# Performance work log

Hardware: AMD Instinct MI355X
Metric: run time of the kernel (lower is better)

The kernel has to match this reference:

```python
import jax, jax.numpy as jnp
import numpy as np

N = 50000   # nodes
E = 1000000 # edges
D_IN = 64
D_OUT = 64
R = 16      # relations (num_rels == num_bases)


def setup_inputs() -> dict:
    key = jax.random.key(0)
    k1, k2, k3, k4, k5, k6, k7 = jax.random.split(key, 7)
    node_features = jax.random.normal(k1, (N, D_IN), dtype=jnp.float32)
    edge_src = jax.random.randint(k2, (E,), 0, N, dtype=jnp.int32)
    edge_dst = jax.random.randint(k3, (E,), 0, N, dtype=jnp.int32)
    edge_type = jax.random.randint(k4, (E,), 0, R, dtype=jnp.int32)
    edge_norm = jax.random.uniform(k5, (E,), dtype=jnp.float32)
    weight = jax.random.normal(k6, (R, D_IN, D_OUT), dtype=jnp.float32) * 0.1
    bias = jax.random.normal(k7, (D_OUT,), dtype=jnp.float32) * 0.1
    return {
        "node_features": node_features,
        "edge_src": edge_src,
        "edge_dst": edge_dst,
        "edge_type": edge_type,
        "edge_norm": edge_norm,
        "weight": weight,
        "bias": bias,
    }


def reference(node_features, edge_src, edge_dst, edge_type, edge_norm, weight, bias):
    # gather source features and per-edge relation weight matrices
    h_src = node_features[edge_src]              # [E, D_IN]
    w = weight[edge_type]                        # [E, D_IN, D_OUT]
    # per-edge bmm: [E,1,D_IN] @ [E,D_IN,D_OUT] -> [E,D_OUT]
    msg = jnp.einsum('ed,edo->eo', h_src, w)
    msg = msg * edge_norm[:, None]               # norm scaling
    # scatter-sum aggregation over destination nodes
    node_repr = jax.ops.segment_sum(msg, edge_dst, num_segments=N)  # [N, D_OUT]
    node_repr = node_repr + bias
    return jax.nn.relu(node_repr)
```

## Files before the change

kernel.cpp:

```cpp
#include <hip/hip_runtime.h>
#include <hip/hip_bf16.h>


#define NN 50000
#define EE 1000000
#define RR 16
#define NBLK 256
#define EPB 3907
#define BSH 6
#define NBUK 782
#define NS (NBUK * NBLK)
#define SCAP 2048

typedef __attribute__((ext_vector_type(8))) short short8;
typedef __attribute__((ext_vector_type(4))) float f32x4;

static __device__ inline unsigned short f2bf(float f) {
  union { __hip_bfloat16 h; unsigned short u; } cv;
  cv.h = __float2bfloat16(f);
  return cv.u;
}
static __device__ inline float bf2f(unsigned short u) {
  union { unsigned i; float f; } cv;
  cv.i = ((unsigned)u) << 16;
  return cv.f;
}

__global__ __launch_bounds__(256) void k_wt(const float* __restrict__ W,
                                            unsigned short* __restrict__ Wt) {
  __shared__ __align__(16) unsigned short Wl[64][72];
  const int r = blockIdx.x, tid = threadIdx.x;
  for (int i = tid; i < 4096; i += 256) Wl[i & 63][i >> 6] = f2bf(W[(r << 12) + i]);
  __syncthreads();
  const int o = tid >> 2, kc = (tid & 3) << 4;
  const short8 v0 = *reinterpret_cast<const short8*>(&Wl[o][kc]);
  const short8 v1 = *reinterpret_cast<const short8*>(&Wl[o][kc + 8]);
  unsigned short* dst = Wt + (r << 12) + (o << 6) + kc;
  *reinterpret_cast<short8*>(dst) = v0;
  *reinterpret_cast<short8*>(dst + 8) = v1;
}

__global__ __launch_bounds__(256) void k_gemm_hist(const float* __restrict__ nf,
                                                   const unsigned short* __restrict__ Wt,
                                                   const int* __restrict__ edst,
                                                   unsigned short* __restrict__ X,
                                                   int* __restrict__ cntT) {
  __shared__ __align__(16) char smem[4 * 64 * 72 * 2];
  const int bid = blockIdx.x, tid = threadIdx.x;
  if (bid < NBLK) {
    int* cnt = reinterpret_cast<int*>(smem);
    for (int i = tid; i < NBUK; i += 256) cnt[i] = 0;
    __syncthreads();
    const int e0 = bid * EPB, e1 = min(EE, e0 + EPB);
    for (int e = e0 + tid; e < e1; e += 256) atomicAdd(&cnt[edst[e] >> BSH], 1);
    __syncthreads();
    for (int i = tid; i < NBUK; i += 256) cntT[i * NBLK + bid] = cnt[i];
    return;
  }
  auto Wl = reinterpret_cast<unsigned short(*)[64][72]>(smem);
  const int g = bid - NBLK;
  const int bx = g >> 2, r0 = (g & 3) << 2;
  const int lane = tid & 63, wv = tid >> 6;
  const int lr = lane & 15, lg = lane >> 4;
  const int node = (bx << 6) + (wv << 4) + lr;
  #pragma unroll
  for (int rr = 0; rr < 4; ++rr) {
    const unsigned short* src = Wt + (((size_t)(r0 + rr)) << 12) + (tid << 4);
    const short8 v0 = *reinterpret_cast<const short8*>(src);
    const short8 v1 = *reinterpret_cast<const short8*>(src + 8);
    unsigned short* dst = &Wl[rr][tid >> 2][(tid & 3) << 4];
    *reinterpret_cast<short8*>(dst) = v0;
    *reinterpret_cast<short8*>(dst + 8) = v1;
  }
  short8 bf0, bf1;
  if (node < NN) {
    const float* ap = nf + (size_t)node * 64 + lg * 8;
    float4 v0 = *reinterpret_cast<const float4*>(ap);
    float4 v1 = *reinterpret_cast<const float4*>(ap + 4);
    float4 v2 = *reinterpret_cast<const float4*>(ap + 32);
    float4 v3 = *reinterpret_cast<const float4*>(ap + 36);
    bf0 = short8{(short)f2bf(v0.x), (short)f2bf(v0.y), (short)f2bf(v0.z), (short)f2bf(v0.w),
                 (short)f2bf(v1.x), (short)f2bf(v1.y), (short)f2bf(v1.z), (short)f2bf(v1.w)};
    bf1 = short8{(short)f2bf(v2.x), (short)f2bf(v2.y), (short)f2bf(v2.z), (short)f2bf(v2.w),
                 (short)f2bf(v3.x), (short)f2bf(v3.y), (short)f2bf(v3.z), (short)f2bf(v3.w)};
  } else {
    bf0 = short8{0, 0, 0, 0, 0, 0, 0, 0};
    bf1 = bf0;
  }
  __syncthreads();
  #pragma unroll
  for (int rr = 0; rr < 4; ++rr) {
    const int r = r0 + rr;
    short8 a[8];
    #pragma unroll
    for (int c = 0; c < 4; ++c) {
      a[2 * c] = *reinterpret_cast<const short8*>(&Wl[rr][(c << 4) + lr][lg << 3]);
      a[2 * c + 1] = *reinterpret_cast<const short8*>(&Wl[rr][(c << 4) + lr][32 + (lg << 3)]);
    }
    f32x4 acc[4];
    #pragma unroll
    for (int c = 0; c < 4; ++c) {
      acc[c] = f32x4{0.f, 0.f, 0.f, 0.f};
      acc[c] = __builtin_amdgcn_mfma_f32_16x16x32_bf16(a[2 * c], bf0, acc[c], 0, 0, 0);
      acc[c] = __builtin_amdgcn_mfma_f32_16x16x32_bf16(a[2 * c + 1], bf1, acc[c], 0, 0, 0);
    }
    if (node < NN) {
      #pragma unroll
      for (int c = 0; c < 4; ++c) {
        uint2 p;
        p.x = (unsigned)f2bf(acc[c][0]) | ((unsigned)f2bf(acc[c][1]) << 16);
        p.y = (unsigned)f2bf(acc[c][2]) | ((unsigned)f2bf(acc[c][3]) << 16);
        *reinterpret_cast<uint2*>(&X[((size_t)r * NN + node) * 64 + (c << 4) + (lg << 2)]) = p;
      }
    }
  }
}

__global__ __launch_bounds__(256) void k_scan_a(const int* __restrict__ cntT,
                                                int* __restrict__ offsT,
                                                int* __restrict__ bsum) {
  __shared__ int s[256];
  const int t = threadIdx.x;
  const int i = blockIdx.x * 256 + t;
  const int v = cntT[i];
  s[t] = v;
  __syncthreads();
  #pragma unroll
  for (int off = 1; off < 256; off <<= 1) {
    const int x = (t >= off) ? s[t - off] : 0;
    __syncthreads();
    s[t] += x;
    __syncthreads();
  }
  offsT[i] = s[t] - v;
  if (t == 255) bsum[blockIdx.x] = s[255];
}

__global__ __launch_bounds__(1024) void k_scan_b(const int* __restrict__ bsum,
                                                 int* __restrict__ bsum2) {
  __shared__ int s[1024];
  const int t = threadIdx.x;
  const int v = (t < NBUK) ? bsum[t] : 0;
  s[t] = v;
  __syncthreads();
  #pragma unroll
  for (int off = 1; off < 1024; off <<= 1) {
    const int x = (t >= off) ? s[t - off] : 0;
    __syncthreads();
    s[t] += x;
    __syncthreads();
  }
  if (t < NBUK) bsum2[t] = s[t] - v;
  if (t == NBUK) bsum2[NBUK] = EE;
}

__global__ __launch_bounds__(256) void k_scatter(const int* __restrict__ esrc,
                                                 const int* __restrict__ edst,
                                                 const int* __restrict__ etyp,
                                                 const float* __restrict__ enorm,
                                                 const int* __restrict__ offsT,
                                                 const int* __restrict__ bsum2,
                                                 uint2* __restrict__ rec) {
  __shared__ int cur[NBUK];
  const int bl = blockIdx.x, tid = threadIdx.x;
  for (int i = tid; i < NBUK; i += 256) cur[i] = offsT[i * NBLK + bl] + bsum2[i];
  __syncthreads();
  const int e0 = bl * EPB, e1 = min(EE, e0 + EPB);
  for (int e = e0 + tid; e < e1; e += 256) {
    const int d = edst[e];
    const int pos = atomicAdd(&cur[d >> BSH], 1);
    rec[pos] = make_uint2(((unsigned)(etyp[e] * NN + esrc[e]) << 6) | (unsigned)(d & 63),
                          __float_as_uint(enorm[e]));
  }
}

__global__ __launch_bounds__(256) void k_nsort(const int* __restrict__ bsum2,
                                               uint2* __restrict__ rec,
                                               int* __restrict__ noffs) {
  __shared__ uint2 sbuf[SCAP];
  __shared__ int cnt[64], cur[64];
  const int bu = blockIdx.x, tid = threadIdx.x;
  const int s = bsum2[bu];
  const int e = bsum2[bu + 1];
  const int n = e - s;
  if (tid < 64) cnt[tid] = 0;
  __syncthreads();
  if (n > SCAP) {
    if (tid < 64) noffs[(bu << BSH) + tid] = -1;
    return;
  }
  for (int i = tid; i < n; i += 256) {
    const uint2 r = rec[s + i];
    sbuf[i] = r;
    atomicAdd(&cnt[r.x & 63u], 1);
  }
  __syncthreads();
  if (tid < 64) {
    const int v = cnt[tid];
    int x = v;
    #pragma unroll
    for (int off = 1; off < 64; off <<= 1) {
      const int t = __shfl_up(x, off, 64);
      if (tid >= off) x += t;
    }
    cur[tid] = x - v;
    noffs[(bu << BSH) + tid] = s + x - v;
  }
  __syncthreads();
  for (int i = tid; i < n; i += 256) {
    const uint2 r = sbuf[i];
    const int pos = atomicAdd(&cur[r.x & 63u], 1);
    rec[s + pos] = r;
  }
}

__global__ __launch_bounds__(256) void k_ngather(const uint2* __restrict__ rec,
                                                 const int* __restrict__ noffs,
                                                 const int* __restrict__ bsum2,
                                                 const unsigned short* __restrict__ X,
                                                 const float* __restrict__ bias,
                                                 float* __restrict__ out) {
  const int w = (int)((blockIdx.x * 256 + threadIdx.x) >> 6);
  const int lane = threadIdx.x & 63;
  if (w >= NN) return;
  const int quarter = lane >> 4, d4 = lane & 15;
  const int bu = w >> BSH;
  float4 acc = {0.f, 0.f, 0.f, 0.f};
  const int jb = noffs[w];
  if (jb >= 0) {
    const int je = ((w & 63) == 63) ? bsum2[bu + 1] : noffs[w + 1];
    for (int base = jb; base < je; base += 64) {
      const int deg = min(64, je - base);
      unsigned rxs = 0;
      float rns = 0.f;
      if (lane < deg) {
        const uint2 r = rec[base + lane];
        rxs = r.x >> 6;
        rns = __uint_as_float(r.y);
      }
      int u = 0;
      for (; u + 8 <= deg; u += 8) {
        const int i0 = u + quarter, i1 = u + 4 + quarter;
        const unsigned row0 = (unsigned)__shfl((int)rxs, i0, 64);
        const float n0 = __shfl(rns, i0, 64);
        const unsigned row1 = (unsigned)__shfl((int)rxs, i1, 64);
        const float n1 = __shfl(rns, i1, 64);
        const uint2 x0 = *reinterpret_cast<const uint2*>(X + (size_t)row0 * 64 + (d4 << 2));
        const uint2 x1 = *reinterpret_cast<const uint2*>(X + (size_t)row1 * 64 + (d4 << 2));
        acc.x = fmaf(n0, bf2f((unsigned short)(x0.x & 0xffffu)), acc.x);
        acc.y = fmaf(n0, bf2f((unsigned short)(x0.x >> 16)), acc.y);
        acc.z = fmaf(n0, bf2f((unsigned short)(x0.y & 0xffffu)), acc.z);
        acc.w = fmaf(n0, bf2f((unsigned short)(x0.y >> 16)), acc.w);
        acc.x = fmaf(n1, bf2f((unsigned short)(x1.x & 0xffffu)), acc.x);
        acc.y = fmaf(n1, bf2f((unsigned short)(x1.x >> 16)), acc.y);
        acc.z = fmaf(n1, bf2f((unsigned short)(x1.y & 0xffffu)), acc.z);
        acc.w = fmaf(n1, bf2f((unsigned short)(x1.y >> 16)), acc.w);
      }
      for (; u < deg; u += 4) {
        const int i = u + quarter;
        const int ic = min(i, deg - 1);
        const unsigned row = (unsigned)__shfl((int)rxs, ic, 64);
        float n = __shfl(rns, ic, 64);
        n = (i < deg) ? n : 0.f;
        const uint2 x = *reinterpret_cast<const uint2*>(X + (size_t)row * 64 + (d4 << 2));
        acc.x = fmaf(n, bf2f((unsigned short)(x.x & 0xffffu)), acc.x);
        acc.y = fmaf(n, bf2f((unsigned short)(x.x >> 16)), acc.y);
        acc.z = fmaf(n, bf2f((unsigned short)(x.y & 0xffffu)), acc.z);
        acc.w = fmaf(n, bf2f((unsigned short)(x.y >> 16)), acc.w);
      }
    }
  } else {
    if (quarter == 0) {
      const int s = bsum2[bu];
      const int e = bsum2[bu + 1];
      const unsigned dl = (unsigned)(w & 63);
      for (int j = s; j < e; ++j) {
        const uint2 r = rec[j];
        if ((r.x & 63u) == dl) {
          const float n = __uint_as_float(r.y);
          const uint2 x =
              *reinterpret_cast<const uint2*>(X + (size_t)(r.x >> 6) * 64 + (d4 << 2));
          acc.x = fmaf(n, bf2f((unsigned short)(x.x & 0xffffu)), acc.x);
          acc.y = fmaf(n, bf2f((unsigned short)(x.x >> 16)), acc.y);
          acc.z = fmaf(n, bf2f((unsigned short)(x.y & 0xffffu)), acc.z);
          acc.w = fmaf(n, bf2f((unsigned short)(x.y >> 16)), acc.w);
        }
      }
    }
  }
  acc.x += __shfl_xor(acc.x, 16, 64);
  acc.y += __shfl_xor(acc.y, 16, 64);
  acc.z += __shfl_xor(acc.z, 16, 64);
  acc.w += __shfl_xor(acc.w, 16, 64);
  acc.x += __shfl_xor(acc.x, 32, 64);
  acc.y += __shfl_xor(acc.y, 32, 64);
  acc.z += __shfl_xor(acc.z, 32, 64);
  acc.w += __shfl_xor(acc.w, 32, 64);
  if (quarter == 0) {
    const float4 b = reinterpret_cast<const float4*>(bias)[d4];
    float4 o;
    o.x = fmaxf(acc.x + b.x, 0.f);
    o.y = fmaxf(acc.y + b.y, 0.f);
    o.z = fmaxf(acc.z + b.z, 0.f);
    o.w = fmaxf(acc.w + b.w, 0.f);
    reinterpret_cast<float4*>(out)[(size_t)w * 16 + d4] = o;
  }
}

extern "C" void kernel_launch(void* const* d_in, const int* in_sizes, int n_in,
                              void* d_out, int out_size, void* d_ws, size_t ws_size,
                              hipStream_t stream) {
  const float* nf = (const float*)d_in[0];
  const int* esrc = (const int*)d_in[1];
  const int* edst = (const int*)d_in[2];
  const int* etyp = (const int*)d_in[3];
  const float* enorm = (const float*)d_in[4];
  const float* W = (const float*)d_in[5];
  const float* bias = (const float*)d_in[6];
  float* out = (float*)d_out;

  char* ws = (char*)d_ws;
  unsigned short* X = (unsigned short*)ws;
  unsigned short* Wt = (unsigned short*)(ws + 102400000);
  uint2* rec = (uint2*)(ws + 102531072);
  int* cntT = (int*)(ws + 110531072);
  int* offsT = (int*)(ws + 111331840);
  int* bsum = (int*)(ws + 112132608);
  int* bsum2 = (int*)(ws + 112135736);
  int* noffs = (int*)(ws + 112138868);

  k_wt<<<RR, 256, 0, stream>>>(W, Wt);
  k_gemm_hist<<<NBLK + NBUK * 4, 256, 0, stream>>>(nf, Wt, edst, X, cntT);
  k_scan_a<<<NS / 256, 256, 0, stream>>>(cntT, offsT, bsum);
  k_scan_b<<<1, 1024, 0, stream>>>(bsum, bsum2);
  k_scatter<<<NBLK, 256, 0, stream>>>(esrc, edst, etyp, enorm, offsT, bsum2, rec);
  k_nsort<<<NBUK, 256, 0, stream>>>(bsum2, rec, noffs);
  k_ngather<<<(NN * 64 + 255) / 256, 256, 0, stream>>>(rec, noffs, bsum2, X, bias, out);
}
```

Baseline: 103.2 us.

## Fuse per-bucket node sort and gather into one shared-memory kernel

Merges the bucket counting sort and the per-node gather into a single kernel with 1024-thread blocks, one block per 64-node bucket. Sorted edge records stay in shared memory instead of being written back to global memory and re-read, and node offsets live in shared memory instead of a global array. This removes one launch and a global round-trip of the record array. The gather loop also gains a 16-edge unrolled path with four independent loads in flight. In exchange, each block holds more shared memory and only 782 large blocks run, which may reduce occupancy and parallelism in the gather phase.

```diff
diff --git a/kernel.cpp b/kernel.cpp
--- a/kernel.cpp
+++ b/kernel.cpp
@@ -174,136 +174,150 @@
   }
 }
 
-__global__ __launch_bounds__(256) void k_nsort(const int* __restrict__ bsum2,
-                                               uint2* __restrict__ rec,
-                                               int* __restrict__ noffs) {
+__global__ __launch_bounds__(1024) void k_sortgather(const int* __restrict__ bsum2,
+                                                     const uint2* __restrict__ rec,
+                                                     const unsigned short* __restrict__ X,
+                                                     const float* __restrict__ bias,
+                                                     float* __restrict__ out) {
   __shared__ uint2 sbuf[SCAP];
-  __shared__ int cnt[64], cur[64];
+  __shared__ uint2 sbuf2[SCAP];
+  __shared__ int cnt[64], cur[64], nstart[65];
   const int bu = blockIdx.x, tid = threadIdx.x;
   const int s = bsum2[bu];
   const int e = bsum2[bu + 1];
   const int n = e - s;
+  const int lane = tid & 63, wv = tid >> 6;
+  const int quarter = lane >> 4, d4 = lane & 15;
   if (tid < 64) cnt[tid] = 0;
   __syncthreads();
-  if (n > SCAP) {
-    if (tid < 64) noffs[(bu << BSH) + tid] = -1;
-    return;
-  }
-  for (int i = tid; i < n; i += 256) {
-    const uint2 r = rec[s + i];
-    sbuf[i] = r;
-    atomicAdd(&cnt[r.x & 63u], 1);
-  }
-  __syncthreads();
-  if (tid < 64) {
-    const int v = cnt[tid];
-    int x = v;
-    #pragma unroll
-    for (int off = 1; off < 64; off <<= 1) {
-      const int t = __shfl_up(x, off, 64);
-      if (tid >= off) x += t;
-    }
-    cur[tid] = x - v;
-    noffs[(bu << BSH) + tid] = s + x - v;
-  }
-  __syncthreads();
-  for (int i = tid; i < n; i += 256) {
-    const uint2 r = sbuf[i];
-    const int pos = atomicAdd(&cur[r.x & 63u], 1);
-    rec[s + pos] = r;
-  }
-}
-
-__global__ __launch_bounds__(256) void k_ngather(const uint2* __restrict__ rec,
-                                                 const int* __restrict__ noffs,
-                                                 const int* __restrict__ bsum2,
-                                                 const unsigned short* __restrict__ X,
-                                                 const float* __restrict__ bias,
-                                                 float* __restrict__ out) {
-  const int w = (int)((blockIdx.x * 256 + threadIdx.x) >> 6);
-  const int lane = threadIdx.x & 63;
-  if (w >= NN) return;
-  const int quarter = lane >> 4, d4 = lane & 15;
-  const int bu = w >> BSH;
-  float4 acc = {0.f, 0.f, 0.f, 0.f};
-  const int jb = noffs[w];
-  if (jb >= 0) {
-    const int je = ((w & 63) == 63) ? bsum2[bu + 1] : noffs[w + 1];
-    for (int base = jb; base < je; base += 64) {
-      const int deg = min(64, je - base);
-      unsigned rxs = 0;
-      float rns = 0.f;
-      if (lane < deg) {
-        const uint2 r = rec[base + lane];
-        rxs = r.x >> 6;
-        rns = __uint_as_float(r.y);
+  const bool sorted = (n <= SCAP);
+  if (sorted) {
+    for (int i = tid; i < n; i += 1024) {
+      const uint2 r = rec[s + i];
+      sbuf[i] = r;
+      atomicAdd(&cnt[r.x & 63u], 1);
+    }
+    __syncthreads();
+    if (tid < 64) {
+      const int v = cnt[tid];
+      int x = v;
+      #pragma unroll
+      for (int off = 1; off < 64; off <<= 1) {
+        const int t = __shfl_up(x, off, 64);
+        if (tid >= off) x += t;
       }
-      int u = 0;
-      for (; u + 8 <= deg; u += 8) {
-        const int i0 = u + quarter, i1 = u + 4 + quarter;
-        const unsigned row0 = (unsigned)__shfl((int)rxs, i0, 64);
-        const float n0 = __shfl(rns, i0, 64);
-        const unsigned row1 = (unsigned)__shfl((int)rxs, i1, 64);
-        const float n1 = __shfl(rns, i1, 64);
-        const uint2 x0 = *reinterpret_cast<const uint2*>(X + (size_t)row0 * 64 + (d4 << 2));
-        const uint2 x1 = *reinterpret_cast<const uint2*>(X + (size_t)row1 * 64 + (d4 << 2));
-        acc.x = fmaf(n0, bf2f((unsigned short)(x0.x & 0xffffu)), acc.x);
-        acc.y = fmaf(n0, bf2f((unsigned short)(x0.x >> 16)), acc.y);
-        acc.z = fmaf(n0, bf2f((unsigned short)(x0.y & 0xffffu)), acc.z);
-        acc.w = fmaf(n0, bf2f((unsigned short)(x0.y >> 16)), acc.w);
-        acc.x = fmaf(n1, bf2f((unsigned short)(x1.x & 0xffffu)), acc.x);
-        acc.y = fmaf(n1, bf2f((unsigned short)(x1.x >> 16)), acc.y);
-        acc.z = fmaf(n1, bf2f((unsigned short)(x1.y & 0xffffu)), acc.z);
-        acc.w = fmaf(n1, bf2f((unsigned short)(x1.y >> 16)), acc.w);
+      cur[tid] = x - v;
+      nstart[tid] = x - v;
+      if (tid == 63) nstart[64] = n;
+    }
+    __syncthreads();
+    for (int i = tid; i < n; i += 1024) {
+      const uint2 r = sbuf[i];
+      const int pos = atomicAdd(&cur[r.x & 63u], 1);
+      sbuf2[pos] = r;
+    }
+    __syncthreads();
+  }
+  #pragma unroll
+  for (int k = 0; k < 4; ++k) {
+    const int nl = (wv << 2) + k;
+    const int w = (bu << BSH) + nl;
+    float4 acc = {0.f, 0.f, 0.f, 0.f};
+    if (sorted) {
+      const int jb = nstart[nl], je = nstart[nl + 1];
+      for (int base = jb; base < je; base += 64) {
+        const int deg = min(64, je - base);
+        unsigned rxs = 0;
+        float rns = 0.f;
+        if (lane < deg) {
+          const uint2 r = sbuf2[base + lane];
+          rxs = r.x >> 6;
+          rns = __uint_as_float(r.y);
+        }
+        int u = 0;
+        for (; u + 16 <= deg; u += 16) {
+          unsigned row[4];
+          float nm[4];
+          uint2 xv[4];
+          #pragma unroll
+          for (int q = 0; q < 4; ++q) {
+            const int i = u + 4 * q + quarter;
+            row[q] = (unsigned)__shfl((int)rxs, i, 64);
+            nm[q] = __shfl(rns, i, 64);
+          }
+          #pragma unroll
+          for (int q = 0; q < 4; ++q)
+            xv[q] = *reinterpret_cast<const uint2*>(X + (size_t)row[q] * 64 + (d4 << 2));
+          #pragma unroll
+          for (int q = 0; q < 4; ++q) {
+            acc.x = fmaf(nm[q], bf2f((unsigned short)(xv[q].x & 0xffffu)), acc.x);
+            acc.y = fmaf(nm[q], bf2f((unsigned short)(xv[q].x >> 16)), acc.y);
+            acc.z = fmaf(nm[q], bf2f((unsigned short)(xv[q].y & 0xffffu)), acc.z);
+            acc.w = fmaf(nm[q], bf2f((unsigned short)(xv[q].y >> 16)), acc.w);
+          }
+        }
+        for (; u + 8 <= deg; u += 8) {
+          const int i0 = u + quarter, i1 = u + 4 + quarter;
+          const unsigned row0 = (unsigned)__shfl((int)rxs, i0, 64);
+          const float n0 = __shfl(rns, i0, 64);
+          const unsigned row1 = (unsigned)__shfl((int)rxs, i1, 64);
+          const float n1 = __shfl(rns, i1, 64);
+          const uint2 x0 = *reinterpret_cast<const uint2*>(X + (size_t)row0 * 64 + (d4 << 2));
+          const uint2 x1 = *reinterpret_cast<const uint2*>(X + (size_t)row1 * 64 + (d4 << 2));
+          acc.x = fmaf(n0, bf2f((unsigned short)(x0.x & 0xffffu)), acc.x);
+          acc.y = fmaf(n0, bf2f((unsigned short)(x0.x >> 16)), acc.y);
+          acc.z = fmaf(n0, bf2f((unsigned short)(x0.y & 0xffffu)), acc.z);
+          acc.w = fmaf(n0, bf2f((unsigned short)(x0.y >> 16)), acc.w);
+          acc.x = fmaf(n1, bf2f((unsigned short)(x1.x & 0xffffu)), acc.x);
+          acc.y = fmaf(n1, bf2f((unsigned short)(x1.x >> 16)), acc.y);
+          acc.z = fmaf(n1, bf2f((unsigned short)(x1.y & 0xffffu)), acc.z);
+          acc.w = fmaf(n1, bf2f((unsigned short)(x1.y >> 16)), acc.w);
+        }
+        for (; u < deg; u += 4) {
+          const int i = u + quarter;
+          const int ic = min(i, deg - 1);
+          const unsigned row = (unsigned)__shfl((int)rxs, ic, 64);
+          float nm = __shfl(rns, ic, 64);
+          nm = (i < deg) ? nm : 0.f;
+          const uint2 x = *reinterpret_cast<const uint2*>(X + (size_t)row * 64 + (d4 << 2));
+          acc.x = fmaf(nm, bf2f((unsigned short)(x.x & 0xffffu)), acc.x);
+          acc.y = fmaf(nm, bf2f((unsigned short)(x.x >> 16)), acc.y);
+          acc.z = fmaf(nm, bf2f((unsigned short)(x.y & 0xffffu)), acc.z);
+          acc.w = fmaf(nm, bf2f((unsigned short)(x.y >> 16)), acc.w);
+        }
       }
-      for (; u < deg; u += 4) {
-        const int i = u + quarter;
-        const int ic = min(i, deg - 1);
-        const unsigned row = (unsigned)__shfl((int)rxs, ic, 64);
-        float n = __shfl(rns, ic, 64);
-        n = (i < deg) ? n : 0.f;
-        const uint2 x = *reinterpret_cast<const uint2*>(X + (size_t)row * 64 + (d4 << 2));
-        acc.x = fmaf(n, bf2f((unsigned short)(x.x & 0xffffu)), acc.x);
-        acc.y = fmaf(n, bf2f((unsigned short)(x.x >> 16)), acc.y);
-        acc.z = fmaf(n, bf2f((unsigned short)(x.y & 0xffffu)), acc.z);
-        acc.w = fmaf(n, bf2f((unsigned short)(x.y >> 16)), acc.w);
-      }
-    }
-  } else {
-    if (quarter == 0) {
-      const int s = bsum2[bu];
-      const int e = bsum2[bu + 1];
-      const unsigned dl = (unsigned)(w & 63);
+    } else if (quarter == 0) {
+      const unsigned dl = (unsigned)nl;
       for (int j = s; j < e; ++j) {
         const uint2 r = rec[j];
         if ((r.x & 63u) == dl) {
-          const float n = __uint_as_float(r.y);
+          const float nm = __uint_as_float(r.y);
           const uint2 x =
               *reinterpret_cast<const uint2*>(X + (size_t)(r.x >> 6) * 64 + (d4 << 2));
-          acc.x = fmaf(n, bf2f((unsigned short)(x.x & 0xffffu)), acc.x);
-          acc.y = fmaf(n, bf2f((unsigned short)(x.x >> 16)), acc.y);
-          acc.z = fmaf(n, bf2f((unsigned short)(x.y & 0xffffu)), acc.z);
-          acc.w = fmaf(n, bf2f((unsigned short)(x.y >> 16)), acc.w);
+          acc.x = fmaf(nm, bf2f((unsigned short)(x.x & 0xffffu)), acc.x);
+          acc.y = fmaf(nm, bf2f((unsigned short)(x.x >> 16)), acc.y);
+          acc.z = fmaf(nm, bf2f((unsigned short)(x.y & 0xffffu)), acc.z);
+          acc.w = fmaf(nm, bf2f((unsigned short)(x.y >> 16)), acc.w);
         }
       }
     }
-  }
-  acc.x += __shfl_xor(acc.x, 16, 64);
-  acc.y += __shfl_xor(acc.y, 16, 64);
-  acc.z += __shfl_xor(acc.z, 16, 64);
-  acc.w += __shfl_xor(acc.w, 16, 64);
-  acc.x += __shfl_xor(acc.x, 32, 64);
-  acc.y += __shfl_xor(acc.y, 32, 64);
-  acc.z += __shfl_xor(acc.z, 32, 64);
-  acc.w += __shfl_xor(acc.w, 32, 64);
-  if (quarter == 0) {
-    const float4 b = reinterpret_cast<const float4*>(bias)[d4];
-    float4 o;
-    o.x = fmaxf(acc.x + b.x, 0.f);
-    o.y = fmaxf(acc.y + b.y, 0.f);
-    o.z = fmaxf(acc.z + b.z, 0.f);
-    o.w = fmaxf(acc.w + b.w, 0.f);
-    reinterpret_cast<float4*>(out)[(size_t)w * 16 + d4] = o;
+    acc.x += __shfl_xor(acc.x, 16, 64);
+    acc.y += __shfl_xor(acc.y, 16, 64);
+    acc.z += __shfl_xor(acc.z, 16, 64);
+    acc.w += __shfl_xor(acc.w, 16, 64);
+    acc.x += __shfl_xor(acc.x, 32, 64);
+    acc.y += __shfl_xor(acc.y, 32, 64);
+    acc.z += __shfl_xor(acc.z, 32, 64);
+    acc.w += __shfl_xor(acc.w, 32, 64);
+    if (quarter == 0 && w < NN) {
+      const float4 b = reinterpret_cast<const float4*>(bias)[d4];
+      float4 o;
+      o.x = fmaxf(acc.x + b.x, 0.f);
+      o.y = fmaxf(acc.y + b.y, 0.f);
+      o.z = fmaxf(acc.z + b.z, 0.f);
+      o.w = fmaxf(acc.w + b.w, 0.f);
+      reinterpret_cast<float4*>(out)[(size_t)w * 16 + d4] = o;
+    }
   }
 }
 
@@ -327,13 +341,11 @@
   int* offsT = (int*)(ws + 111331840);
   int* bsum = (int*)(ws + 112132608);
   int* bsum2 = (int*)(ws + 112135736);
-  int* noffs = (int*)(ws + 112138868);
 
   k_wt<<<RR, 256, 0, stream>>>(W, Wt);
   k_gemm_hist<<<NBLK + NBUK * 4, 256, 0, stream>>>(nf, Wt, edst, X, cntT);
   k_scan_a<<<NS / 256, 256, 0, stream>>>(cntT, offsT, bsum);
   k_scan_b<<<1, 1024, 0, stream>>>(bsum, bsum2);
   k_scatter<<<NBLK, 256, 0, stream>>>(esrc, edst, etyp, enorm, offsT, bsum2, rec);
-  k_nsort<<<NBUK, 256, 0, stream>>>(bsum2, rec, noffs);
-  k_ngather<<<(NN * 64 + 255) / 256, 256, 0, stream>>>(rec, noffs, bsum2, X, bias, out);
-}
+  k_sortgather<<<NBUK, 1024, 0, stream>>>(bsum2, rec, X, bias, out);
+}
```

Measured after the change: 95.45 us, median of 2. 1.08x faster.
